# Kernel tuning notes

Measured on AMD Instinct MI355X. Metric: run time of the kernel, lower is better.

## Reference

```python
import jax, jax.numpy as jnp
import numpy as np

B, T, V, C = 256, 2048, 32000, 128  # batch, chars, vocab_len, out_channels


def setup_inputs() -> dict:
    key = jax.random.key(0)
    k_idx, k_w, k_b = jax.random.split(key, 3)
    inputs = jax.random.randint(k_idx, (B, 1, T), 0, V)  # (Batch, 1, Chars) int ids
    # nn.Linear(vocab_len, out_channels): weight (C, V), bias (C,)
    bound = 1.0 / np.sqrt(V)
    W = jax.random.uniform(k_w, (C, V), dtype=jnp.float32, minval=-bound, maxval=bound)
    b = jax.random.uniform(k_b, (C,), dtype=jnp.float32, minval=-bound, maxval=bound)
    return {"inputs": inputs, "W": W, "b": b}


def reference(inputs, W, b):
    # one_hot(inputs) @ W.T + b  ==  gather rows of W.T at the indices, + b.
    # This is exactly the same math as the torch module (scatter one-hot then Linear),
    # without materializing the (B, V, T) one-hot tensor.
    idx = inputs[:, 0, :]                 # (B, T)
    emb = jnp.take(W.T, idx, axis=0)      # (B, T, C)
    out = emb + b                         # broadcast bias over (B, T)
    return jnp.transpose(out, (0, 2, 1))  # (B, C, T) to match torch output permute
```

## Files before the change

kernel.cpp:

```cpp
#include <hip/hip_runtime.h>

#define B_ 256
#define T_ 2048
#define V_ 32000
#define C_ 128

typedef float v4f __attribute__((ext_vector_type(4)));
typedef int   v4i __attribute__((ext_vector_type(4)));

__global__ __launch_bounds__(256) void transpose_bias_kernel(
    const float* __restrict__ W, const float* __restrict__ bias,
    float* __restrict__ Wt) {
    __shared__ float tile[32][33];
    const int v0 = blockIdx.x * 32;
    const int c0 = blockIdx.y * 32;
    const int tx = threadIdx.x;
    const int ty = threadIdx.y;
#pragma unroll
    for (int i = 0; i < 4; ++i) {
        const int cl = ty + i * 8;
        tile[cl][tx] = __builtin_nontemporal_load(
            W + (size_t)(c0 + cl) * V_ + v0 + tx);
    }
    __syncthreads();
#pragma unroll
    for (int i = 0; i < 4; ++i) {
        const int vl = ty + i * 8;
        const int c  = c0 + tx;
        Wt[(size_t)(v0 + vl) * C_ + c] = tile[tx][vl] + bias[c];
    }
}

__global__ __launch_bounds__(256) void gather_kernel(
    const int* __restrict__ idx, const v4f* __restrict__ Wt4,
    float* __restrict__ out) {
    const int b   = blockIdx.y;
    const int t0  = blockIdx.x * 32;
    const int tid = threadIdx.x;
    const int cq  = tid >> 3;
    const int tg  = tid & 7;
    const int t   = t0 + tg * 4;

    const v4i iv = *(const v4i*)(idx + b * T_ + t);

    const v4f w0 = Wt4[iv.x * (C_ / 4) + cq];
    const v4f w1 = Wt4[iv.y * (C_ / 4) + cq];
    const v4f w2 = Wt4[iv.z * (C_ / 4) + cq];
    const v4f w3 = Wt4[iv.w * (C_ / 4) + cq];

    float* o = out + ((size_t)(b * C_ + cq * 4)) * T_ + t;
    __builtin_nontemporal_store((v4f){w0.x, w1.x, w2.x, w3.x}, (v4f*)(o));
    __builtin_nontemporal_store((v4f){w0.y, w1.y, w2.y, w3.y}, (v4f*)(o + T_));
    __builtin_nontemporal_store((v4f){w0.z, w1.z, w2.z, w3.z}, (v4f*)(o + 2 * T_));
    __builtin_nontemporal_store((v4f){w0.w, w1.w, w2.w, w3.w}, (v4f*)(o + 3 * T_));
}

__global__ __launch_bounds__(256) void gather_direct_kernel(
    const int* __restrict__ idx, const float* __restrict__ W,
    const float* __restrict__ bias, float* __restrict__ out) {
    const size_t o = (size_t)blockIdx.x * blockDim.x + threadIdx.x;
    const int T4   = T_ / 4;
    const int t4   = (int)(o % T4);
    const int rest = (int)(o / T4);
    const int c    = rest % C_;
    const int b    = rest / C_;
    const v4i iv   = *(const v4i*)(idx + (size_t)b * T_ + (size_t)t4 * 4);
    const float* Wr = W + (size_t)c * V_;
    const float bc  = bias[c];
    __builtin_nontemporal_store(
        (v4f){Wr[iv.x] + bc, Wr[iv.y] + bc, Wr[iv.z] + bc, Wr[iv.w] + bc},
        ((v4f*)out) + o);
}

extern "C" void kernel_launch(void* const* d_in, const int* in_sizes, int n_in,
                              void* d_out, int out_size, void* d_ws, size_t ws_size,
                              hipStream_t stream) {
    const int*   idx  = (const int*)d_in[0];
    const float* W    = (const float*)d_in[1];
    const float* bias = (const float*)d_in[2];
    float*       out  = (float*)d_out;

    const size_t wt_bytes = (size_t)V_ * C_ * sizeof(float);

    if (ws_size >= wt_bytes) {
        float* Wt = (float*)d_ws;
        transpose_bias_kernel<<<dim3(V_ / 32, C_ / 32), dim3(32, 8), 0, stream>>>(
            W, bias, Wt);
        gather_kernel<<<dim3(T_ / 32, B_), 256, 0, stream>>>(
            idx, (const v4f*)Wt, out);
    } else {
        const size_t total = (size_t)B_ * C_ * (T_ / 4);
        gather_direct_kernel<<<(unsigned)((total + 255) / 256), 256, 0, stream>>>(
            idx, W, bias, out);
    }
}
```

Baseline: 304.9 us.

## Stage transposed weights in output tail and fill tail batches directly

The transposed-plus-bias weight table is now stored in the last 16 batches of the output buffer instead of the workspace. The main gather kernel covers only the first 240 batches. A new tail kernel then overwrites the scratch region with those batches, reading the original W rows directly and keeping the indices in shared memory. This drops the dependence on workspace size and may improve cache locality, but the tail kernel does strided gathers from untransposed W and adds a third launch.

```diff
diff --git a/kernel.cpp b/kernel.cpp
--- a/kernel.cpp
+++ b/kernel.cpp
@@ -4,6 +4,8 @@
 #define T_ 2048
 #define V_ 32000
 #define C_ 128
+
+#define TAIL_B 240
 
 typedef float v4f __attribute__((ext_vector_type(4)));
 typedef int   v4i __attribute__((ext_vector_type(4)));
@@ -55,21 +57,37 @@
     __builtin_nontemporal_store((v4f){w0.w, w1.w, w2.w, w3.w}, (v4f*)(o + 3 * T_));
 }
 
-__global__ __launch_bounds__(256) void gather_direct_kernel(
+__global__ __launch_bounds__(256) void tail_kernel(
     const int* __restrict__ idx, const float* __restrict__ W,
     const float* __restrict__ bias, float* __restrict__ out) {
-    const size_t o = (size_t)blockIdx.x * blockDim.x + threadIdx.x;
-    const int T4   = T_ / 4;
-    const int t4   = (int)(o % T4);
-    const int rest = (int)(o / T4);
-    const int c    = rest % C_;
-    const int b    = rest / C_;
-    const v4i iv   = *(const v4i*)(idx + (size_t)b * T_ + (size_t)t4 * 4);
+    __shared__ int tIdx[T_];
+    const int c  = blockIdx.x;
+    const int b  = TAIL_B + blockIdx.y;
+    const int tid = threadIdx.x;
+
+    const v4i* idx4 = (const v4i*)(idx + (size_t)b * T_);
+#pragma unroll
+    for (int k = 0; k < 2; ++k) {
+        ((v4i*)tIdx)[tid + k * 256] = idx4[tid + k * 256];
+    }
+    __syncthreads();
+
     const float* Wr = W + (size_t)c * V_;
     const float bc  = bias[c];
-    __builtin_nontemporal_store(
-        (v4f){Wr[iv.x] + bc, Wr[iv.y] + bc, Wr[iv.z] + bc, Wr[iv.w] + bc},
-        ((v4f*)out) + o);
+    float* orow = out + ((size_t)b * C_ + c) * T_;
+
+    const int t0 = tid * 8;
+    v4f r0, r1;
+    r0.x = Wr[tIdx[t0 + 0]] + bc;
+    r0.y = Wr[tIdx[t0 + 1]] + bc;
+    r0.z = Wr[tIdx[t0 + 2]] + bc;
+    r0.w = Wr[tIdx[t0 + 3]] + bc;
+    r1.x = Wr[tIdx[t0 + 4]] + bc;
+    r1.y = Wr[tIdx[t0 + 5]] + bc;
+    r1.z = Wr[tIdx[t0 + 6]] + bc;
+    r1.w = Wr[tIdx[t0 + 7]] + bc;
+    __builtin_nontemporal_store(r0, (v4f*)(orow + t0));
+    __builtin_nontemporal_store(r1, (v4f*)(orow + t0 + 4));
 }
 
 extern "C" void kernel_launch(void* const* d_in, const int* in_sizes, int n_in,
@@ -80,17 +98,12 @@
     const float* bias = (const float*)d_in[2];
     float*       out  = (float*)d_out;
 
-    const size_t wt_bytes = (size_t)V_ * C_ * sizeof(float);
+    float* Wt = out + (size_t)TAIL_B * C_ * T_;
 
-    if (ws_size >= wt_bytes) {
-        float* Wt = (float*)d_ws;
-        transpose_bias_kernel<<<dim3(V_ / 32, C_ / 32), dim3(32, 8), 0, stream>>>(
-            W, bias, Wt);
-        gather_kernel<<<dim3(T_ / 32, B_), 256, 0, stream>>>(
-            idx, (const v4f*)Wt, out);
-    } else {
-        const size_t total = (size_t)B_ * C_ * (T_ / 4);
-        gather_direct_kernel<<<(unsigned)((total + 255) / 256), 256, 0, stream>>>(
-            idx, W, bias, out);
-    }
+    transpose_bias_kernel<<<dim3(V_ / 32, C_ / 32), dim3(32, 8), 0, stream>>>(
+        W, bias, Wt);
+    gather_kernel<<<dim3(T_ / 32, TAIL_B), 256, 0, stream>>>(
+        idx, (const v4f*)Wt, out);
+    tail_kernel<<<dim3(C_, B_ - TAIL_B), 256, 0, stream>>>(
+        idx, W, bias, out);
 }
```

Result: slower. 324.7 us (+6.5%).

## Slice gather by channel groups so consecutive blocks share a slice of Wt

Applied to the files above, without the earlier changes.

The gather kernel now uses a 1D grid in which the low 3 bits of the block id select one of 8 channel slices (16 channels each). Each block covers 256 time steps for one batch row, and each wave writes 64 contiguous time steps across 4 channel quads. This makes each block's stores wider per output row and concentrates the gathered Wt reads on a 64-byte slice per vocabulary row. In exchange, the idx loads are repeated across the 8 slice blocks and each Wt row is fetched in smaller pieces.

```diff
diff --git a/kernel.cpp b/kernel.cpp
--- a/kernel.cpp
+++ b/kernel.cpp
@@ -31,24 +31,31 @@
     }
 }
 
-__global__ __launch_bounds__(256) void gather_kernel(
+__global__ __launch_bounds__(256) void gather_sliced_kernel(
     const int* __restrict__ idx, const v4f* __restrict__ Wt4,
     float* __restrict__ out) {
-    const int b   = blockIdx.y;
-    const int t0  = blockIdx.x * 32;
+    const int bid   = blockIdx.x;
+    const int slice = bid & 7;
+    const int rest  = bid >> 3;
+    const int b     = rest & (B_ - 1);
+    const int t0    = (rest >> 8) * 256;
+
     const int tid = threadIdx.x;
-    const int cq  = tid >> 3;
-    const int tg  = tid & 7;
-    const int t   = t0 + tg * 4;
+    const int w   = tid >> 6;
+    const int l   = tid & 63;
+    const int cq  = l & 3;
+    const int tg  = l >> 2;
+    const int t   = t0 + w * 64 + tg * 4;
 
     const v4i iv = *(const v4i*)(idx + b * T_ + t);
 
-    const v4f w0 = Wt4[iv.x * (C_ / 4) + cq];
-    const v4f w1 = Wt4[iv.y * (C_ / 4) + cq];
-    const v4f w2 = Wt4[iv.z * (C_ / 4) + cq];
-    const v4f w3 = Wt4[iv.w * (C_ / 4) + cq];
+    const int cbase = slice * 4 + cq;
+    const v4f w0 = Wt4[iv.x * (C_ / 4) + cbase];
+    const v4f w1 = Wt4[iv.y * (C_ / 4) + cbase];
+    const v4f w2 = Wt4[iv.z * (C_ / 4) + cbase];
+    const v4f w3 = Wt4[iv.w * (C_ / 4) + cbase];
 
-    float* o = out + ((size_t)(b * C_ + cq * 4)) * T_ + t;
+    float* o = out + ((size_t)(b * C_ + cbase * 4)) * T_ + t;
     __builtin_nontemporal_store((v4f){w0.x, w1.x, w2.x, w3.x}, (v4f*)(o));
     __builtin_nontemporal_store((v4f){w0.y, w1.y, w2.y, w3.y}, (v4f*)(o + T_));
     __builtin_nontemporal_store((v4f){w0.z, w1.z, w2.z, w3.z}, (v4f*)(o + 2 * T_));
@@ -86,7 +93,7 @@
         float* Wt = (float*)d_ws;
         transpose_bias_kernel<<<dim3(V_ / 32, C_ / 32), dim3(32, 8), 0, stream>>>(
             W, bias, Wt);
-        gather_kernel<<<dim3(T_ / 32, B_), 256, 0, stream>>>(
+        gather_sliced_kernel<<<dim3(8 * B_ * (T_ / 256)), 256, 0, stream>>>(
             idx, (const v4f*)Wt, out);
     } else {
         const size_t total = (size_t)B_ * C_ * (T_ / 4);
```

New measurement: 301.0 us. Within noise of the previous version (-1.3%).
